# Kernel optimization log

Measured on AMD Instinct MI355X. Metric: run time of the kernel, lower is better.

Reference implementation:

```python
import jax, jax.numpy as jnp
import numpy as np

V, H, B, S = 128, 512, 512, 256


def setup_inputs() -> dict:
    key = jax.random.key(0)
    ks = jax.random.split(key, 12)
    s = 0.02
    inp = {
        'x': jax.random.randint(ks[0], (B, S), 0, V),
        # gate order: i, f, o, g (candidate)
        'Wx_f': jax.random.normal(ks[1], (4, H, V), jnp.float32) * s,
        'Wh_f': jax.random.normal(ks[2], (4, H, H), jnp.float32) * s,
        'bx_f': jnp.zeros((4, H), jnp.float32),
        'bh_f': jnp.zeros((4, H), jnp.float32),
        'Wx_b': jax.random.normal(ks[3], (4, H, V), jnp.float32) * s,
        'Wh_b': jax.random.normal(ks[4], (4, H, H), jnp.float32) * s,
        'bx_b': jnp.zeros((4, H), jnp.float32),
        'bh_b': jnp.zeros((4, H), jnp.float32),
        'Wfc': jax.random.normal(ks[5], (V, 2 * H), jnp.float32) * s,
        'bfc': jnp.zeros((V,), jnp.float32),
    }
    return inp


def _lstm_scan(xoh, Wx, Wh, bx, bh):
    # xoh: [S, B, V]; Wx: [4, H, V]; Wh: [4, H, H]
    b = xoh.shape[1]
    h0 = jnp.zeros((b, Wh.shape[-1]), xoh.dtype)
    c0 = jnp.zeros_like(h0)
    # precompute input contribution for all timesteps: one GEMM
    gx = jnp.einsum('sbv,ghv->sgbh', xoh, Wx) + bx[None, :, None, :]  # [S,4,B,H]

    def step(carry, gxt):
        h, c = carry
        g = gxt + jnp.einsum('bh,gkh->gbk', h, Wh) + bh[:, None, :]  # [4,B,H]
        i = jax.nn.sigmoid(g[0])
        f = jax.nn.sigmoid(g[1])
        o = jax.nn.sigmoid(g[2])
        gg = jnp.tanh(g[3])
        c = f * c + i * gg
        h = o * jnp.tanh(c)
        return (h, c), h

    _, hs = jax.lax.scan(step, (h0, c0), gx)
    return hs  # [S, B, H]


def reference(x, Wx_f, Wh_f, bx_f, bh_f, Wx_b, Wh_b, bx_b, bh_b, Wfc, bfc):
    xoh = jax.nn.one_hot(x, V, dtype=jnp.float32)           # [B,S,V]
    xoh = jnp.transpose(xoh, (1, 0, 2))                      # [S,B,V]
    hf = _lstm_scan(xoh, Wx_f, Wh_f, bx_f, bh_f)             # [S,B,H]
    hb = _lstm_scan(xoh[::-1], Wx_b, Wh_b, bx_b, bh_b)[::-1] # [S,B,H]
    comb = jnp.concatenate([hf, hb], axis=-1)                # [S,B,2H]
    y = jnp.einsum('sbh,vh->sbv', comb, Wfc) + bfc           # [S,B,V]
    return jnp.transpose(y, (1, 0, 2))                       # [B,S,V]
```

## Files before the change

kernel.cpp:

```cpp
#include <hip/hip_runtime.h>

#define Hd 512
#define Bd 512
#define Vd 128
#define Sd 256

typedef _Float16 half8 __attribute__((ext_vector_type(8)));
typedef _Float16 half4v __attribute__((ext_vector_type(4)));
typedef float float4v __attribute__((ext_vector_type(4)));
typedef unsigned int uint4v __attribute__((ext_vector_type(4)));

__device__ __forceinline__ float sigf(float v) { return 1.0f / (1.0f + __expf(-v)); }
__device__ __forceinline__ float tanhfast(float v) { return 1.0f - 2.0f / (__expf(2.0f * v) + 1.0f); }

__device__ __forceinline__ void load_lds16(const void* g, void* l) {
  __builtin_amdgcn_global_load_lds(
      (const __attribute__((address_space(1))) unsigned int*)g,
      (__attribute__((address_space(3))) unsigned int*)l, 16, 0, 0);
}

#if __has_builtin(__builtin_amdgcn_raw_buffer_load_b128) && \
    __has_builtin(__builtin_amdgcn_make_buffer_rsrc)
#define USE_BUFLD 1
#else
#define USE_BUFLD 0
#endif

#if USE_BUFLD
__device__ __forceinline__ half8 load_frag(__amdgpu_buffer_rsrc_t rs,
                                           const _Float16* base, unsigned voff) {
  uint4v d = __builtin_amdgcn_raw_buffer_load_b128(rs, voff, 0, 1 );
  union { uint4v u; half8 h; } cv; cv.u = d;
  return cv.h;
}
#else
typedef int __amdgpu_buffer_rsrc_t;
__device__ __forceinline__ half8 load_frag(__amdgpu_buffer_rsrc_t rs,
                                           const _Float16* base, unsigned voff) {
  (void)rs;
  const char* p = (const char*)base + voff;
  union { unsigned long long u[2]; half8 h; } cv;
  cv.u[0] = __hip_atomic_load((const unsigned long long*)p, __ATOMIC_RELAXED,
                              __HIP_MEMORY_SCOPE_AGENT);
  cv.u[1] = __hip_atomic_load((const unsigned long long*)(p + 8), __ATOMIC_RELAXED,
                              __HIP_MEMORY_SCOPE_AGENT);
  return cv.h;
}
#endif

__device__ __forceinline__ void storeh4(_Float16* base, unsigned voff, half4v v) {
  *(half4v*)((char*)base + voff) = v;
}

__global__ __launch_bounds__(256) void prep_wxt(
    const float* __restrict__ WxF, const float* __restrict__ bxF, const float* __restrict__ bhF,
    const float* __restrict__ WxB, const float* __restrict__ bxB, const float* __restrict__ bhB,
    float* __restrict__ wxt) {
  int e = blockIdx.x * 256 + threadIdx.x;
  int n = e & 2047;
  int v = (e >> 11) & 127;
  int dir = e >> 18;
  int k = n >> 2, g = n & 3;
  const float* Wx = dir ? WxB : WxF;
  const float* bx = dir ? bxB : bxF;
  const float* bh = dir ? bhB : bhF;
  int gk = g * Hd + k;
  wxt[e] = Wx[gk * Vd + v] + bx[gk] + bh[gk];
}

__global__ __launch_bounds__(256) void prep_wh16(
    const float* __restrict__ WhF, const float* __restrict__ WhB, _Float16* __restrict__ whr) {
  int e = blockIdx.x * 256 + threadIdx.x;
  int hc = e & 511;
  int n = (e >> 9) & 2047;
  int dir = e >> 20;
  int k = n >> 2, g = n & 3;
  const float* Wh = dir ? WhB : WhF;
  whr[e] = (_Float16)Wh[(g * Hd + k) * Hd + hc];
}

__global__ __launch_bounds__(256) void prep_wfc16(
    const float* __restrict__ Wfc, _Float16* __restrict__ wfc16) {
  int e = blockIdx.x * 256 + threadIdx.x;
  int hc = e & 511;
  int v = (e >> 9) & 127;
  int dir = e >> 16;
  wfc16[e] = (_Float16)Wfc[v * 1024 + dir * 512 + hc];
}

__global__ __launch_bounds__(256) void prep_xT(const int* __restrict__ x, int* __restrict__ xT) {
  int e = blockIdx.x * 256 + threadIdx.x;
  int t = e >> 9, b = e & 511;
  xT[e] = x[b * Sd + t];
}

__global__ __launch_bounds__(256) void init_zero(float* __restrict__ p) {
  int e = blockIdx.x * 256 + threadIdx.x;
  float4 z; z.x = 0.f; z.y = 0.f; z.z = 0.f; z.w = 0.f;
  ((float4*)p)[e] = z;
}

__global__ __launch_bounds__(256) void init_out(const float* __restrict__ bfc,
                                                float* __restrict__ out) {
  int e = blockIdx.x * 256 + threadIdx.x;
  int v0 = (e & 31) * 4;
  ((float4*)out)[e] = *(const float4*)&bfc[v0];
}

#define SMEM_BYTES (131072 + 17408)

#define ISSUE2(D, C)                                                           \
  _Pragma("unroll") for (int j = 0; j < 2; ++j)                                \
      D[j] = load_frag(rs, hbuf, aoff + (unsigned)(((C) * 2 + j) * 1024));

#define COMPUTE2(D, C)                                                         \
  _Pragma("unroll") for (int j = 0; j < 2; ++j) {                              \
    const int kcabs = ks * 8 + (C) * 2 + j;                                    \
    _Pragma("unroll") for (int ni = 0; ni < 8; ++ni) {                         \
      half8 bf = *(const half8*)((const char*)smem + brow[ni] +                \
                                 (((kcabs * 4 + kq) ^ bxor[ni]) * 16));        \
      acc[ni] = __builtin_amdgcn_mfma_f32_16x16x32_f16(D[j], bf, acc[ni], 0, 0, 0); \
    }                                                                          \
  }

#define FCC(D, C)                                                              \
  _Pragma("unroll") for (int j = 0; j < 2; ++j)                                \
      fa = __builtin_amdgcn_mfma_f32_16x16x32_f16(                             \
          D[j], *(const half8*)(Bfc + ((C) * 2 + j) * 32), fa, 0, 0, 0);

__global__ __launch_bounds__(512, 1) void bilstm_persist(
    const float* __restrict__ wxt, const int* __restrict__ xT,
    const _Float16* __restrict__ whr, const _Float16* __restrict__ wfc16,
    _Float16* __restrict__ hbuf, unsigned* __restrict__ flags,
    float* __restrict__ out) {
  extern __shared__ char smem[];
  _Float16* GT = (_Float16*)(smem + 131072);

  const int tid = threadIdx.x;
  const int lane = tid & 63;
  const int w = tid >> 6;
  const int ks = w >> 2;
  const int wl = w & 3;

  unsigned xcd;
  asm volatile("s_getreg_b32 %0, hwreg(HW_REG_XCC_ID)" : "=s"(xcd));
  xcd &= 7u;
  unsigned* xcdctr = flags + 8176;
  int* roleSh = (int*)GT;
  if (tid == 0) roleSh[0] = (int)atomicAdd(&xcdctr[xcd], 1u);
  __syncthreads();
  const int rank = roleSh[0];
  const int grp = (int)xcd * 2 + (rank >> 4);
  const int nt = rank & 15;
  const int dir = grp >> 3;
  const int mt = grp & 7;
  const int b0 = mt * 64;
  __syncthreads();

  {
    const char* wsrc = (const char*)(whr + ((size_t)(dir * 2048 + nt * 128)) * Hd);
#pragma unroll
    for (int i = 0; i < 16; ++i) {
      int e = i * 512 + tid;
      int n = e >> 6, cs = e & 63;
      load_lds16(wsrc + (size_t)n * 1024 + (size_t)(((cs ^ (n & 7)) * 16)),
                 (char*)smem + (size_t)e * 16);
    }
  }

  const int l15 = lane & 15;
  const int kq = lane >> 4;

#if USE_BUFLD
  const __amdgpu_buffer_rsrc_t rs = __builtin_amdgcn_make_buffer_rsrc(
      (void*)hbuf, (short)0, (int)4194304, 0x00020000);
#else
  const __amdgpu_buffer_rsrc_t rs = 0;
#endif

  const unsigned aoff_lane = (unsigned)((b0 >> 4) + wl) * 16384u + kq * 256u +
                             l15 * 16u + (unsigned)ks * 8192u;

  int brow[8], bxor[8];
#pragma unroll
  for (int ni = 0; ni < 8; ++ni) {
    int n = ni * 16 + l15;
    brow[ni] = n * 1024;
    bxor[ni] = n & 7;
  }

  float creg[4];
#pragma unroll
  for (int i = 0; i < 4; ++i) creg[i] = 0.f;

  const int bl = tid & 63;
  const int kh = tid >> 6;
  const int fcn = nt & 7;
  const int gtm = wl * 16 + kq * 4;
  const unsigned soff_lane = (unsigned)(((b0 + bl) >> 4)) * 16384u +
                             (unsigned)(nt * 4 + (kh >> 1)) * 256u +
                             (unsigned)(bl & 15) * 16u + (unsigned)(kh & 1) * 8u;

  __syncthreads();

  for (int s = 0; s <= Sd; ++s) {
    const unsigned abase = (((unsigned)(s & 3)) * 2u + (unsigned)dir) * 524288u;
    const unsigned nbase = (((unsigned)(s + 1) & 3u) * 2u + (unsigned)dir) * 524288u;
    const unsigned aoff = abase + aoff_lane;

    half8 a0[2], a1[2], a2[2], a3[2];

    if (s < Sd) {
      float4v acc[8];
#pragma unroll
      for (int ni = 0; ni < 8; ++ni) acc[ni] = (float4v)0.f;

      ISSUE2(a0, 0)
      ISSUE2(a1, 1)
      ISSUE2(a2, 2)
      COMPUTE2(a0, 0)
      ISSUE2(a3, 3)
      COMPUTE2(a1, 1)
      COMPUTE2(a2, 2)
      COMPUTE2(a3, 3)

      const int t = dir ? (Sd - 1 - s) : s;
      const int b = b0 + bl;
      const int xv = xT[t * Bd + b];
      const float* wrow = wxt + ((size_t)(dir * Vd + xv)) * 2048 + nt * 128 + kh * 16;
      float4 wv[4];
#pragma unroll
      for (int kl = 0; kl < 4; ++kl) wv[kl] = *(const float4*)&wrow[kl * 4];

      if (ks == 1) {
#pragma unroll
        for (int ni = 0; ni < 8; ++ni) {
          int n = ni * 16 + l15;
          half4v hv4;
          hv4[0] = (_Float16)acc[ni][0];
          hv4[1] = (_Float16)acc[ni][1];
          hv4[2] = (_Float16)acc[ni][2];
          hv4[3] = (_Float16)acc[ni][3];
          *(half4v*)&GT[n * 68 + gtm] = hv4;
        }
      }
      __syncthreads();
      if (ks == 0) {
#pragma unroll
        for (int ni = 0; ni < 8; ++ni) {
          int n = ni * 16 + l15;
          half4v g4 = *(half4v*)&GT[n * 68 + gtm];
          half4v hv4;
          hv4[0] = (_Float16)(acc[ni][0] + (float)g4[0]);
          hv4[1] = (_Float16)(acc[ni][1] + (float)g4[1]);
          hv4[2] = (_Float16)(acc[ni][2] + (float)g4[2]);
          hv4[3] = (_Float16)(acc[ni][3] + (float)g4[3]);
          *(half4v*)&GT[n * 68 + gtm] = hv4;
        }
      }
      __syncthreads();

      half4v hv;
#pragma unroll
      for (int kl = 0; kl < 4; ++kl) {
        int kloc = kh * 4 + kl;
        float g0 = (float)GT[(kloc * 4 + 0) * 68 + bl] + wv[kl].x;
        float g1 = (float)GT[(kloc * 4 + 1) * 68 + bl] + wv[kl].y;
        float g2 = (float)GT[(kloc * 4 + 2) * 68 + bl] + wv[kl].z;
        float g3 = (float)GT[(kloc * 4 + 3) * 68 + bl] + wv[kl].w;
        float gi = sigf(g0), gf = sigf(g1), go = sigf(g2), gg = tanhfast(g3);
        float cn = gf * creg[kl] + gi * gg;
        creg[kl] = cn;
        hv[kl] = (_Float16)(go * tanhfast(cn));
      }
      storeh4(hbuf, nbase + soff_lane, hv);

      __syncthreads();
      if (tid == 0)
        __hip_atomic_store(&flags[(grp * 16 + nt) * 32], (unsigned)(s + 1),
                           __ATOMIC_RELAXED, __HIP_MEMORY_SCOPE_AGENT);
    } else {
      ISSUE2(a0, 0)
      ISSUE2(a1, 1)
      ISSUE2(a2, 2)
      ISSUE2(a3, 3)
    }

    const bool fc_act = (s & 1) ? (nt < 8) : (nt >= 8);
    if (s > 0 && fc_act) {
      const _Float16* Bfc = wfc16 + (size_t)dir * (Vd * Hd) +
                            (size_t)(fcn * 16 + l15) * Hd + ks * 256 + kq * 8;
      float4v fa = (float4v)0.f;
      FCC(a0, 0)
      FCC(a1, 1)
      FCC(a2, 2)
      FCC(a3, 3)
      const int tf = dir ? (Sd - s) : (s - 1);
      const int v = fcn * 16 + l15;
      const int bb = b0 + wl * 16 + kq * 4;
      float* op = out + ((size_t)bb * Sd + tf) * Vd + v;
#pragma unroll
      for (int r2 = 0; r2 < 4; ++r2)
        unsafeAtomicAdd(op + (size_t)r2 * (Sd * Vd), fa[r2]);
    }

    if (s == Sd) break;

    if (tid < 16) {
      unsigned* f = flags + (grp * 16 + tid) * 32;
      while (__hip_atomic_load(f, __ATOMIC_RELAXED, __HIP_MEMORY_SCOPE_AGENT) <
             (unsigned)(s + 1))
        __builtin_amdgcn_s_sleep(1);
    }
    __syncthreads();
  }
}

extern "C" void kernel_launch(void* const* d_in, const int* in_sizes, int n_in,
                              void* d_out, int out_size, void* d_ws, size_t ws_size,
                              hipStream_t stream) {
  (void)in_sizes; (void)n_in; (void)out_size; (void)ws_size;
  const int* x      = (const int*)d_in[0];
  const float* WxF  = (const float*)d_in[1];
  const float* WhF  = (const float*)d_in[2];
  const float* bxF  = (const float*)d_in[3];
  const float* bhF  = (const float*)d_in[4];
  const float* WxB  = (const float*)d_in[5];
  const float* WhB  = (const float*)d_in[6];
  const float* bxB  = (const float*)d_in[7];
  const float* bhB  = (const float*)d_in[8];
  const float* Wfc  = (const float*)d_in[9];
  const float* bfc  = (const float*)d_in[10];
  float* out = (float*)d_out;

  float* ws = (float*)d_ws;
  float* wxt        = ws;
  _Float16* hbuf    = (_Float16*)(ws + 524288);
  unsigned* flags   = (unsigned*)(ws + 1572864);
  _Float16* wh16    = (_Float16*)(ws + 1581056);
  _Float16* wfc16   = (_Float16*)(ws + 2629632);
  int* xT           = (int*)(ws + 2695168);

  prep_wxt<<<2048, 256, 0, stream>>>(WxF, bxF, bhF, WxB, bxB, bhB, wxt);
  prep_wh16<<<8192, 256, 0, stream>>>(WhF, WhB, wh16);
  prep_wfc16<<<512, 256, 0, stream>>>(Wfc, wfc16);
  prep_xT<<<512, 256, 0, stream>>>(x, xT);
  init_zero<<<256, 256, 0, stream>>>(ws + 524288);
  init_zero<<<8, 256, 0, stream>>>(ws + 1572864);
  init_out<<<16384, 256, 0, stream>>>(bfc, out);

  static bool attr_set = false;
  if (!attr_set) {
    (void)hipFuncSetAttribute((const void*)bilstm_persist,
                              hipFuncAttributeMaxDynamicSharedMemorySize, SMEM_BYTES);
    attr_set = true;
  }
  void* kargs[] = {(void*)&wxt, (void*)&xT, (void*)&wh16, (void*)&wfc16,
                   (void*)&hbuf, (void*)&flags, (void*)&out};
  if (hipLaunchCooperativeKernel((const void*)bilstm_persist, dim3(256), dim3(512),
                                 kargs, SMEM_BYTES, stream) != hipSuccess) {
    bilstm_persist<<<dim3(256), dim3(512), SMEM_BYTES, stream>>>(
        wxt, xT, wh16, wfc16, hbuf, flags, out);
  }
}
```

Baseline: 1.614 ms.

## Cache recurrent weight fragments in registers, retile waves 2x2, per-wave flag polling

Each wave now loads its slice of the recurrent weight matrix from LDS into registers once, before the time loop, instead of re-reading the B fragments from LDS every step. Waves are retiled so each covers two 16-row M tiles and four 16-column N tiles, which reuses each A fragment across more MFMAs. The FC projection is split across the N-half index to match the new tiling. Every wave now polls the dependency flags itself, replacing the end-of-step block barrier. The register cache greatly raises VGPR pressure and may cause spills or lower occupancy.

Measured after the change: 1.858 ms. 15.1% more time.

```diff
diff --git a/kernel.cpp b/kernel.cpp
--- a/kernel.cpp
+++ b/kernel.cpp
@@ -110,23 +110,22 @@
 #define SMEM_BYTES (131072 + 17408)
 
 #define ISSUE2(D, C)                                                           \
+  _Pragma("unroll") for (int mi = 0; mi < 2; ++mi)                             \
   _Pragma("unroll") for (int j = 0; j < 2; ++j)                                \
-      D[j] = load_frag(rs, hbuf, aoff + (unsigned)(((C) * 2 + j) * 1024));
+      D[mi][j] = load_frag(rs, hbuf, aoff[mi] + (unsigned)(((C) * 2 + j) * 1024));
 
 #define COMPUTE2(D, C)                                                         \
-  _Pragma("unroll") for (int j = 0; j < 2; ++j) {                              \
-    const int kcabs = ks * 8 + (C) * 2 + j;                                    \
-    _Pragma("unroll") for (int ni = 0; ni < 8; ++ni) {                         \
-      half8 bf = *(const half8*)((const char*)smem + brow[ni] +                \
-                                 (((kcabs * 4 + kq) ^ bxor[ni]) * 16));        \
-      acc[ni] = __builtin_amdgcn_mfma_f32_16x16x32_f16(D[j], bf, acc[ni], 0, 0, 0); \
-    }                                                                          \
-  }
+  _Pragma("unroll") for (int j = 0; j < 2; ++j)                                \
+  _Pragma("unroll") for (int mi = 0; mi < 2; ++mi)                             \
+  _Pragma("unroll") for (int ni = 0; ni < 4; ++ni)                             \
+      acc[mi][ni] = __builtin_amdgcn_mfma_f32_16x16x32_f16(                    \
+          D[mi][j], bcache[(C) * 2 + j][ni], acc[mi][ni], 0, 0, 0);
 
 #define FCC(D, C)                                                              \
   _Pragma("unroll") for (int j = 0; j < 2; ++j)                                \
-      fa = __builtin_amdgcn_mfma_f32_16x16x32_f16(                             \
-          D[j], *(const half8*)(Bfc + ((C) * 2 + j) * 32), fa, 0, 0, 0);
+  _Pragma("unroll") for (int mi = 0; mi < 2; ++mi)                             \
+      fa[mi] = __builtin_amdgcn_mfma_f32_16x16x32_f16(                         \
+          D[mi][j], *(const half8*)(Bfc + ((C) * 2 + j) * 32), fa[mi], 0, 0, 0);
 
 __global__ __launch_bounds__(512, 1) void bilstm_persist(
     const float* __restrict__ wxt, const int* __restrict__ xT,
@@ -140,7 +139,8 @@
   const int lane = tid & 63;
   const int w = tid >> 6;
   const int ks = w >> 2;
-  const int wl = w & 3;
+  const int nh = (w >> 1) & 1;
+  const int wl2 = w & 1;
 
   unsigned xcd;
   asm volatile("s_getreg_b32 %0, hwreg(HW_REG_XCC_ID)" : "=s"(xcd));
@@ -178,16 +178,11 @@
   const __amdgpu_buffer_rsrc_t rs = 0;
 #endif
 
-  const unsigned aoff_lane = (unsigned)((b0 >> 4) + wl) * 16384u + kq * 256u +
-                             l15 * 16u + (unsigned)ks * 8192u;
-
-  int brow[8], bxor[8];
-#pragma unroll
-  for (int ni = 0; ni < 8; ++ni) {
-    int n = ni * 16 + l15;
-    brow[ni] = n * 1024;
-    bxor[ni] = n & 7;
-  }
+  unsigned aoff_lane[2];
+#pragma unroll
+  for (int mi = 0; mi < 2; ++mi)
+    aoff_lane[mi] = (unsigned)((b0 >> 4) + wl2 * 2 + mi) * 16384u + kq * 256u +
+                    l15 * 16u + (unsigned)ks * 8192u;
 
   float creg[4];
 #pragma unroll
@@ -196,24 +191,40 @@
   const int bl = tid & 63;
   const int kh = tid >> 6;
   const int fcn = nt & 7;
-  const int gtm = wl * 16 + kq * 4;
   const unsigned soff_lane = (unsigned)(((b0 + bl) >> 4)) * 16384u +
                              (unsigned)(nt * 4 + (kh >> 1)) * 256u +
                              (unsigned)(bl & 15) * 16u + (unsigned)(kh & 1) * 8u;
+  unsigned* pollflag = flags + (grp * 16 + l15) * 32;
 
   __syncthreads();
+
+  half8 bcache[8][4];
+#pragma unroll
+  for (int c = 0; c < 8; ++c) {
+    const int kcabs = ks * 8 + c;
+#pragma unroll
+    for (int ni = 0; ni < 4; ++ni) {
+      const int n = nh * 64 + ni * 16 + l15;
+      bcache[c][ni] = *(const half8*)((const char*)smem + n * 1024 +
+                                      (((kcabs * 4 + kq) ^ (n & 7)) * 16));
+    }
+  }
 
   for (int s = 0; s <= Sd; ++s) {
     const unsigned abase = (((unsigned)(s & 3)) * 2u + (unsigned)dir) * 524288u;
     const unsigned nbase = (((unsigned)(s + 1) & 3u) * 2u + (unsigned)dir) * 524288u;
-    const unsigned aoff = abase + aoff_lane;
-
-    half8 a0[2], a1[2], a2[2], a3[2];
+    unsigned aoff[2];
+    aoff[0] = abase + aoff_lane[0];
+    aoff[1] = abase + aoff_lane[1];
+
+    half8 a0[2][2], a1[2][2], a2[2][2], a3[2][2];
 
     if (s < Sd) {
-      float4v acc[8];
-#pragma unroll
-      for (int ni = 0; ni < 8; ++ni) acc[ni] = (float4v)0.f;
+      float4v acc[2][4];
+#pragma unroll
+      for (int mi = 0; mi < 2; ++mi)
+#pragma unroll
+        for (int ni = 0; ni < 4; ++ni) acc[mi][ni] = (float4v)0.f;
 
       ISSUE2(a0, 0)
       ISSUE2(a1, 1)
@@ -234,28 +245,36 @@
 
       if (ks == 1) {
 #pragma unroll
-        for (int ni = 0; ni < 8; ++ni) {
-          int n = ni * 16 + l15;
-          half4v hv4;
-          hv4[0] = (_Float16)acc[ni][0];
-          hv4[1] = (_Float16)acc[ni][1];
-          hv4[2] = (_Float16)acc[ni][2];
-          hv4[3] = (_Float16)acc[ni][3];
-          *(half4v*)&GT[n * 68 + gtm] = hv4;
+        for (int mi = 0; mi < 2; ++mi) {
+          const int m = wl2 * 32 + mi * 16 + kq * 4;
+#pragma unroll
+          for (int ni = 0; ni < 4; ++ni) {
+            const int n = nh * 64 + ni * 16 + l15;
+            half4v hv4;
+            hv4[0] = (_Float16)acc[mi][ni][0];
+            hv4[1] = (_Float16)acc[mi][ni][1];
+            hv4[2] = (_Float16)acc[mi][ni][2];
+            hv4[3] = (_Float16)acc[mi][ni][3];
+            *(half4v*)&GT[n * 68 + m] = hv4;
+          }
         }
       }
       __syncthreads();
       if (ks == 0) {
 #pragma unroll
-        for (int ni = 0; ni < 8; ++ni) {
-          int n = ni * 16 + l15;
-          half4v g4 = *(half4v*)&GT[n * 68 + gtm];
-          half4v hv4;
-          hv4[0] = (_Float16)(acc[ni][0] + (float)g4[0]);
-          hv4[1] = (_Float16)(acc[ni][1] + (float)g4[1]);
-          hv4[2] = (_Float16)(acc[ni][2] + (float)g4[2]);
-          hv4[3] = (_Float16)(acc[ni][3] + (float)g4[3]);
-          *(half4v*)&GT[n * 68 + gtm] = hv4;
+        for (int mi = 0; mi < 2; ++mi) {
+          const int m = wl2 * 32 + mi * 16 + kq * 4;
+#pragma unroll
+          for (int ni = 0; ni < 4; ++ni) {
+            const int n = nh * 64 + ni * 16 + l15;
+            half4v g4 = *(half4v*)&GT[n * 68 + m];
+            half4v hv4;
+            hv4[0] = (_Float16)(acc[mi][ni][0] + (float)g4[0]);
+            hv4[1] = (_Float16)(acc[mi][ni][1] + (float)g4[1]);
+            hv4[2] = (_Float16)(acc[mi][ni][2] + (float)g4[2]);
+            hv4[3] = (_Float16)(acc[mi][ni][3] + (float)g4[3]);
+            *(half4v*)&GT[n * 68 + m] = hv4;
+          }
         }
       }
       __syncthreads();
@@ -289,30 +308,32 @@
     const bool fc_act = (s & 1) ? (nt < 8) : (nt >= 8);
     if (s > 0 && fc_act) {
       const _Float16* Bfc = wfc16 + (size_t)dir * (Vd * Hd) +
-                            (size_t)(fcn * 16 + l15) * Hd + ks * 256 + kq * 8;
-      float4v fa = (float4v)0.f;
-      FCC(a0, 0)
-      FCC(a1, 1)
-      FCC(a2, 2)
-      FCC(a3, 3)
+                            (size_t)(fcn * 16 + l15) * Hd + ks * 256 + nh * 128 + kq * 8;
+      float4v fa[2];
+      fa[0] = (float4v)0.f;
+      fa[1] = (float4v)0.f;
+      if (nh == 0) { FCC(a0, 0) FCC(a1, 1) }
+      else         { FCC(a2, 0) FCC(a3, 1) }
       const int tf = dir ? (Sd - s) : (s - 1);
       const int v = fcn * 16 + l15;
-      const int bb = b0 + wl * 16 + kq * 4;
-      float* op = out + ((size_t)bb * Sd + tf) * Vd + v;
-#pragma unroll
-      for (int r2 = 0; r2 < 4; ++r2)
-        unsafeAtomicAdd(op + (size_t)r2 * (Sd * Vd), fa[r2]);
+#pragma unroll
+      for (int mi = 0; mi < 2; ++mi) {
+        const int bb = b0 + wl2 * 32 + mi * 16 + kq * 4;
+        float* op = out + ((size_t)bb * Sd + tf) * Vd + v;
+#pragma unroll
+        for (int r2 = 0; r2 < 4; ++r2)
+          unsafeAtomicAdd(op + (size_t)r2 * (Sd * Vd), fa[mi][r2]);
+      }
     }
 
     if (s == Sd) break;
 
-    if (tid < 16) {
-      unsigned* f = flags + (grp * 16 + tid) * 32;
-      while (__hip_atomic_load(f, __ATOMIC_RELAXED, __HIP_MEMORY_SCOPE_AGENT) <
-             (unsigned)(s + 1))
+    if (lane < 16) {
+      while (__hip_atomic_load(pollflag, __ATOMIC_RELAXED,
+                               __HIP_MEMORY_SCOPE_AGENT) < (unsigned)(s + 1))
         __builtin_amdgcn_s_sleep(1);
     }
-    __syncthreads();
+    asm volatile("" ::: "memory");
   }
 }
 
```
